# Optimization experiments

Measured on AMD Instinct MI355X. Metric: run time of the kernel, lower is better.

The kernel has to match this reference:

```python
import jax, jax.numpy as jnp
import numpy as np

B, Q, K, D = 8, 2048, 2048, 64

def setup_inputs() -> dict:
    key = jax.random.key(0)
    kq, kk, kv, kl = jax.random.split(key, 4)
    queries = jax.random.normal(kq, (B, Q, D), dtype=jnp.float32)
    keys = jax.random.normal(kk, (B, K, D), dtype=jnp.float32)
    values = jax.random.normal(kv, (B, K, D), dtype=jnp.float32)
    valid_lens = jax.random.randint(kl, (B,), 1, K + 1)  # at least 1 valid key
    return {"queries": queries, "keys": keys, "values": values, "valid_lens": valid_lens}

def reference(queries, keys, values, valid_lens):
    d = queries.shape[-1]
    # scores: [B, Q, K]
    scores = jnp.einsum("bqd,bkd->bqk", queries, keys) / jnp.sqrt(jnp.float32(d))
    # d2l-style masked softmax: positions >= valid_len get -1e6 before softmax
    kpos = jnp.arange(scores.shape[-1])  # [K]
    mask = kpos[None, None, :] < valid_lens[:, None, None]  # [B,1,K]
    scores = jnp.where(mask, scores, jnp.float32(-1e6))
    attn = jax.nn.softmax(scores, axis=-1)
    # dropout is identity at inference (training=False)
    return jnp.einsum("bqk,bkd->bqd", attn, values)
```

## Files before the change

### kernel.cpp

```cpp
#include <hip/hip_runtime.h>

typedef float    f32x4  __attribute__((ext_vector_type(4)));
typedef float    f32x16 __attribute__((ext_vector_type(16)));
typedef _Float16 half8  __attribute__((ext_vector_type(8)));

constexpr int NB = 8;
constexpr int NQ = 2048;
constexpr int NKEY = 2048;
constexpr int DD = 64;
constexpr int KB = 32;
constexpr int NT = NKEY / KB;
constexpr size_t TILE_BYTES = (size_t)KB * DD * 2;

#define QSCALE (0.125f * 1.44269504088896340736f)

__device__ inline unsigned pkh(float a, float b) {
    return __builtin_bit_cast(unsigned, __builtin_amdgcn_cvt_pkrtz(a, b));
}
__device__ inline int vswz2(int d) {
    return ((d >> 1) & 3) << 4;
}

#define GLL(gp, lp) __builtin_amdgcn_global_load_lds( \
    (const __attribute__((address_space(1))) void*)(gp), \
    (__attribute__((address_space(3))) void*)(lp), 16, 0, 0)

__global__ __launch_bounds__(256) void convert_kv(
    const float* __restrict__ Kp, const float* __restrict__ Vp,
    char* __restrict__ Kh, char* __restrict__ Vt)
{
    __shared__ __align__(16) char vbuf[32 * 144];
    const int g    = blockIdx.x;
    const bool isV = (g >= NB * NT);
    const int bt   = isV ? g - NB * NT : g;
    const int tid  = threadIdx.x;
    const int b = bt >> 6, T = bt & 63;

    const int key = tid >> 3;
    const int dc  = (tid & 7) * 8;
    const float* src = (isV ? Vp : Kp)
                     + ((size_t)b * NKEY + T * KB + key) * DD + dc;
    f32x4 f0 = *(const f32x4*)src;
    f32x4 f1 = *(const f32x4*)(src + 4);
    half8 h;
#pragma unroll
    for (int i = 0; i < 4; ++i) {
        h[i]     = (_Float16)f0[i];
        h[4 + i] = (_Float16)f1[i];
    }

    if (!isV) {
        char* dst = Kh + (size_t)bt * TILE_BYTES;
        *(half8*)(dst + ((key * 128 + dc * 2) ^ ((key & 7) << 4))) = h;
    } else {
        *(half8*)(vbuf + key * 144 + dc * 2) = h;
        __syncthreads();
        const int d  = tid >> 2;
        const int kc = tid & 3;
        half8 o;
#pragma unroll
        for (int j = 0; j < 8; ++j)
            o[j] = *(const _Float16*)(vbuf + (kc * 8 + j) * 144 + d * 2);
        char* dst = Vt + (size_t)bt * TILE_BYTES;
        *(half8*)(dst + d * 64 + ((kc * 16) ^ vswz2(d))) = o;
    }
}

__device__ __forceinline__ void pv_chunk(
    const f32x16& sv, const char* __restrict__ vsm,
    int hi, int ql, int swzq, f32x16& o0, f32x16& o1)
{
    const unsigned w0 = pkh(sv[0],  sv[1]),  w1 = pkh(sv[2],  sv[3]);
    const unsigned w2 = pkh(sv[4],  sv[5]),  w3 = pkh(sv[6],  sv[7]);
    const unsigned w4 = pkh(sv[8],  sv[9]),  w5 = pkh(sv[10], sv[11]);
    const unsigned w6 = pkh(sv[12], sv[13]), w7 = pkh(sv[14], sv[15]);
    const unsigned p0 = __shfl_xor(w0, 32), p1 = __shfl_xor(w1, 32);
    const unsigned p2 = __shfl_xor(w2, 32), p3 = __shfl_xor(w3, 32);
    const unsigned p4 = __shfl_xor(w4, 32), p5 = __shfl_xor(w5, 32);
    const unsigned p6 = __shfl_xor(w6, 32), p7 = __shfl_xor(w7, 32);
    const bool h1 = (hi != 0);
    union { unsigned u[4]; half8 h; } A0, A1;
    A0.u[0] = h1 ? p2 : w0;  A0.u[1] = h1 ? p3 : w1;
    A0.u[2] = h1 ? w2 : p0;  A0.u[3] = h1 ? w3 : p1;
    A1.u[0] = h1 ? p6 : w4;  A1.u[1] = h1 ? p7 : w5;
    A1.u[2] = h1 ? w6 : p4;  A1.u[3] = h1 ? w7 : p5;

    __builtin_amdgcn_s_setprio(1);
#pragma unroll
    for (int t = 0; t < 2; ++t) {
        const int co = t * 32 + hi * 16;
        const half8 vb0 = *(const half8*)(vsm + ql * 64        + (co ^ swzq));
        const half8 vb1 = *(const half8*)(vsm + (32 + ql) * 64 + (co ^ swzq));
        const half8 pa = (t == 0) ? A0.h : A1.h;
        o0 = __builtin_amdgcn_mfma_f32_32x32x16_f16(pa, vb0, o0, 0, 0, 0);
        o1 = __builtin_amdgcn_mfma_f32_32x32x16_f16(pa, vb1, o1, 0, 0, 0);
    }
    __builtin_amdgcn_s_setprio(0);
}

__global__ __launch_bounds__(512, 4) void attn_fused(
    const float* __restrict__ Qp, const char* __restrict__ Kh,
    const char* __restrict__ Vt, const int* __restrict__ VL,
    float* __restrict__ Op)
{
    __shared__ __align__(16) char pool[67584];

    const int tid  = threadIdx.x;
    const int wv   = tid >> 6;
    const int lane = tid & 63;
    const int ql   = lane & 31;
    const int hi   = lane >> 5;

    char* Ksm = pool + wv * 8192;
    char* Vsm = Ksm + 4096;

    const int g  = blockIdx.x;
    const int b  = ((g >> 3) & 7) ^ ((g >> 8) << 2);
    const int qt = (g & 7) | (((g >> 6) & 7) << 3);
    const int qbase = qt * 32;

    const int vlen = VL[b];
    const int numt = (vlen + KB - 1) / KB;

    const float* qsrc = Qp + ((size_t)b * NQ + qbase + ql) * DD;
    half8 qf[4];
#pragma unroll
    for (int c = 0; c < 4; ++c) {
        f32x4 f0 = *(const f32x4*)(qsrc + c * 16 + hi * 8);
        f32x4 f1 = *(const f32x4*)(qsrc + c * 16 + hi * 8 + 4);
        half8 h;
#pragma unroll
        for (int j = 0; j < 4; ++j) {
            h[j]     = (_Float16)(f0[j] * QSCALE);
            h[4 + j] = (_Float16)(f1[j] * QSCALE);
        }
        qf[c] = h;
    }

    f32x16 o0 = {}, o1 = {};
    float mrun = -1e30f, lrun = 0.f;
    const int swzq = vswz2(ql);

    for (int t = wv; t < numt; t += 8) {
        const int kbase = t * KB;
        const char* ksrc = Kh + (size_t)(b * NT + t) * TILE_BYTES + lane * 16;
        const char* vsrc = Vt + (size_t)(b * NT + t) * TILE_BYTES + lane * 16;

        __builtin_amdgcn_sched_barrier(0);
#pragma unroll
        for (int j = 0; j < 4; ++j) GLL(ksrc + j * 1024, Ksm + j * 1024);
#pragma unroll
        for (int j = 0; j < 4; ++j) GLL(vsrc + j * 1024, Vsm + j * 1024);
        asm volatile("s_waitcnt vmcnt(4)" ::: "memory");
        __builtin_amdgcn_sched_barrier(0);

        f32x16 sv = {};
        __builtin_amdgcn_s_setprio(1);
#pragma unroll
        for (int c = 0; c < 4; ++c) {
            const half8 kf = *(const half8*)(Ksm +
                ((ql * 128 + c * 32 + hi * 16) ^ ((ql & 7) << 4)));
            sv = __builtin_amdgcn_mfma_f32_32x32x16_f16(kf, qf[c], sv, 0, 0, 0);
        }
        __builtin_amdgcn_s_setprio(0);

        if (kbase + KB > vlen) {
#pragma unroll
            for (int r = 0; r < 16; ++r) {
                const int krow = (r & 3) + 8 * (r >> 2) + 4 * hi;
                sv[r] = (kbase + krow < vlen) ? sv[r] : -1e30f;
            }
        }

        float mx[16];
#pragma unroll
        for (int r = 0; r < 16; ++r) mx[r] = sv[r];
#pragma unroll
        for (int st = 8; st > 0; st >>= 1)
#pragma unroll
            for (int r = 0; r < st; ++r) mx[r] = fmaxf(mx[r], mx[r + st]);
        float mr = fmaxf(mx[0], __shfl_xor(mx[0], 32));

        if (!__all(mr <= mrun + 8.f)) {
            const float mn = fmaxf(mrun, mr);
            const float alpha = __builtin_amdgcn_exp2f(mrun - mn);
            lrun *= alpha;
            mrun = mn;
#pragma unroll
            for (int r = 0; r < 16; ++r) {
                const int qr = (r & 3) + 8 * (r >> 2) + 4 * hi;
                const float ar = __shfl(alpha, qr);
                o0[r] *= ar;
                o1[r] *= ar;
            }
        }

#pragma unroll
        for (int r = 0; r < 16; ++r)
            sv[r] = __builtin_amdgcn_exp2f(sv[r] - mrun);
        float sx[16];
#pragma unroll
        for (int r = 0; r < 16; ++r) sx[r] = sv[r];
#pragma unroll
        for (int st = 8; st > 0; st >>= 1)
#pragma unroll
            for (int r = 0; r < st; ++r) sx[r] += sx[r + st];
        lrun += sx[0] + __shfl_xor(sx[0], 32);

        asm volatile("s_waitcnt vmcnt(0)" ::: "memory");
        __builtin_amdgcn_sched_barrier(0);
        pv_chunk(sv, Vsm, hi, ql, swzq, o0, o1);
    }

    __syncthreads();
    float* Mb = (float*)(pool + 65536);
    float* Lb = (float*)(pool + 65536 + 1024);
    float (*Obuf)[32][64] = (float (*)[32][64])pool;

    if (hi == 0) { Mb[wv * 32 + ql] = mrun; Lb[wv * 32 + ql] = lrun; }
    __syncthreads();

    float Mtot = -1e30f;
#pragma unroll
    for (int w = 0; w < 8; ++w)
        if (Lb[w * 32 + ql] > 0.f) Mtot = fmaxf(Mtot, Mb[w * 32 + ql]);
    const float wown = (lrun > 0.f) ? __builtin_amdgcn_exp2f(mrun - Mtot) : 0.f;

#pragma unroll
    for (int r = 0; r < 16; ++r) {
        const int qr = (r & 3) + 8 * (r >> 2) + 4 * hi;
        const float wr = __shfl(wown, qr);
        Obuf[wv][qr][ql]      = o0[r] * wr;
        Obuf[wv][qr][ql + 32] = o1[r] * wr;
    }
    __syncthreads();

    {
        const int q  = tid >> 4;
        const int d0 = (tid & 15) * 4;
        float Mq = -1e30f;
#pragma unroll
        for (int w = 0; w < 8; ++w)
            if (Lb[w * 32 + q] > 0.f) Mq = fmaxf(Mq, Mb[w * 32 + q]);
        float Ltot = 0.f;
#pragma unroll
        for (int w = 0; w < 8; ++w) {
            const float lw = Lb[w * 32 + q];
            if (lw > 0.f) Ltot += lw * __builtin_amdgcn_exp2f(Mb[w * 32 + q] - Mq);
        }
        f32x4 acc = {};
#pragma unroll
        for (int w = 0; w < 8; ++w)
            acc += *(const f32x4*)(&Obuf[w][q][d0]);
        const float inv = 1.0f / Ltot;
        f32x4 outv;
#pragma unroll
        for (int j = 0; j < 4; ++j) outv[j] = acc[j] * inv;
        *(f32x4*)(Op + ((size_t)b * NQ + qbase + q) * DD + d0) = outv;
    }
}

extern "C" void kernel_launch(void* const* d_in, const int* in_sizes, int n_in,
                              void* d_out, int out_size, void* d_ws, size_t ws_size,
                              hipStream_t stream) {
    const float* Qp = (const float*)d_in[0];
    const float* Kp = (const float*)d_in[1];
    const float* Vp = (const float*)d_in[2];
    const int*   VL = (const int*)d_in[3];
    float* Op = (float*)d_out;

    char* Kh = (char*)d_ws;
    char* Vt = (char*)d_ws + (size_t)NB * NT * TILE_BYTES;

    hipLaunchKernelGGL(convert_kv, dim3(2 * NB * NT), dim3(256), 0, stream,
                       Kp, Vp, Kh, Vt);
    hipLaunchKernelGGL(attn_fused, dim3(NB * (NQ / 32)), dim3(512), 0, stream,
                       Qp, Kh, Vt, VL, Op);
}
```

Baseline: 31.14 us.

## Pre-layout K/V tiles in MFMA fragment order and load directly to registers

The conversion kernel now writes K and V tiles in the exact per-lane MFMA operand layout. The attention kernel can then load fragments straight from global memory into registers with coalesced 16-byte loads, with no stop in LDS. This removes the global_load_lds staging, the LDS reads, the swizzle arithmetic and the explicit vmcnt waits. In exchange it gives up LDS staging and relies on the compiler to schedule global-load latency against the QK and softmax work.

```diff
diff --git a/kernel.cpp b/kernel.cpp
--- a/kernel.cpp
+++ b/kernel.cpp
@@ -10,20 +10,13 @@
 constexpr int DD = 64;
 constexpr int KB = 32;
 constexpr int NT = NKEY / KB;
-constexpr size_t TILE_BYTES = (size_t)KB * DD * 2;
+constexpr size_t TILE_BYTES = 4096;
 
 #define QSCALE (0.125f * 1.44269504088896340736f)
 
 __device__ inline unsigned pkh(float a, float b) {
     return __builtin_bit_cast(unsigned, __builtin_amdgcn_cvt_pkrtz(a, b));
 }
-__device__ inline int vswz2(int d) {
-    return ((d >> 1) & 3) << 4;
-}
-
-#define GLL(gp, lp) __builtin_amdgcn_global_load_lds( \
-    (const __attribute__((address_space(1))) void*)(gp), \
-    (__attribute__((address_space(3))) void*)(lp), 16, 0, 0)
 
 __global__ __launch_bounds__(256) void convert_kv(
     const float* __restrict__ Kp, const float* __restrict__ Vp,
@@ -50,8 +43,9 @@
     }
 
     if (!isV) {
-        char* dst = Kh + (size_t)bt * TILE_BYTES;
-        *(half8*)(dst + ((key * 128 + dc * 2) ^ ((key & 7) << 4))) = h;
+        char* dst = Kh + (size_t)bt * TILE_BYTES
+                  + (dc >> 4) * 1024 + (((dc >> 3) & 1) * 32 + key) * 16;
+        *(half8*)dst = h;
     } else {
         *(half8*)(vbuf + key * 144 + dc * 2) = h;
         __syncthreads();
@@ -61,14 +55,15 @@
 #pragma unroll
         for (int j = 0; j < 8; ++j)
             o[j] = *(const _Float16*)(vbuf + (kc * 8 + j) * 144 + d * 2);
-        char* dst = Vt + (size_t)bt * TILE_BYTES;
-        *(half8*)(dst + d * 64 + ((kc * 16) ^ vswz2(d))) = o;
-    }
-}
-
-__device__ __forceinline__ void pv_chunk(
-    const f32x16& sv, const char* __restrict__ vsm,
-    int hi, int ql, int swzq, f32x16& o0, f32x16& o1)
+        const int frag = (kc >> 1) * 2 + (d >> 5);
+        char* dst = Vt + (size_t)bt * TILE_BYTES
+                  + frag * 1024 + ((kc & 1) * 32 + (d & 31)) * 16;
+        *(half8*)dst = o;
+    }
+}
+
+__device__ __forceinline__ void pv_frag(
+    const f32x16& sv, const half8 (&vf)[4], int hi, f32x16& o0, f32x16& o1)
 {
     const unsigned w0 = pkh(sv[0],  sv[1]),  w1 = pkh(sv[2],  sv[3]);
     const unsigned w2 = pkh(sv[4],  sv[5]),  w3 = pkh(sv[6],  sv[7]);
@@ -86,15 +81,10 @@
     A1.u[2] = h1 ? w6 : p4;  A1.u[3] = h1 ? w7 : p5;
 
     __builtin_amdgcn_s_setprio(1);
-#pragma unroll
-    for (int t = 0; t < 2; ++t) {
-        const int co = t * 32 + hi * 16;
-        const half8 vb0 = *(const half8*)(vsm + ql * 64        + (co ^ swzq));
-        const half8 vb1 = *(const half8*)(vsm + (32 + ql) * 64 + (co ^ swzq));
-        const half8 pa = (t == 0) ? A0.h : A1.h;
-        o0 = __builtin_amdgcn_mfma_f32_32x32x16_f16(pa, vb0, o0, 0, 0, 0);
-        o1 = __builtin_amdgcn_mfma_f32_32x32x16_f16(pa, vb1, o1, 0, 0, 0);
-    }
+    o0 = __builtin_amdgcn_mfma_f32_32x32x16_f16(A0.h, vf[0], o0, 0, 0, 0);
+    o1 = __builtin_amdgcn_mfma_f32_32x32x16_f16(A0.h, vf[1], o1, 0, 0, 0);
+    o0 = __builtin_amdgcn_mfma_f32_32x32x16_f16(A1.h, vf[2], o0, 0, 0, 0);
+    o1 = __builtin_amdgcn_mfma_f32_32x32x16_f16(A1.h, vf[3], o1, 0, 0, 0);
     __builtin_amdgcn_s_setprio(0);
 }
 
@@ -111,9 +101,6 @@
     const int ql   = lane & 31;
     const int hi   = lane >> 5;
 
-    char* Ksm = pool + wv * 8192;
-    char* Vsm = Ksm + 4096;
-
     const int g  = blockIdx.x;
     const int b  = ((g >> 3) & 7) ^ ((g >> 8) << 2);
     const int qt = (g & 7) | (((g >> 6) & 7) << 3);
@@ -139,29 +126,23 @@
 
     f32x16 o0 = {}, o1 = {};
     float mrun = -1e30f, lrun = 0.f;
-    const int swzq = vswz2(ql);
 
     for (int t = wv; t < numt; t += 8) {
         const int kbase = t * KB;
-        const char* ksrc = Kh + (size_t)(b * NT + t) * TILE_BYTES + lane * 16;
-        const char* vsrc = Vt + (size_t)(b * NT + t) * TILE_BYTES + lane * 16;
-
-        __builtin_amdgcn_sched_barrier(0);
-#pragma unroll
-        for (int j = 0; j < 4; ++j) GLL(ksrc + j * 1024, Ksm + j * 1024);
-#pragma unroll
-        for (int j = 0; j < 4; ++j) GLL(vsrc + j * 1024, Vsm + j * 1024);
-        asm volatile("s_waitcnt vmcnt(4)" ::: "memory");
-        __builtin_amdgcn_sched_barrier(0);
+        const char* kp = Kh + (size_t)(b * NT + t) * TILE_BYTES + lane * 16;
+        const char* vp = Vt + (size_t)(b * NT + t) * TILE_BYTES + lane * 16;
+
+        half8 kf[4], vf[4];
+#pragma unroll
+        for (int c = 0; c < 4; ++c) kf[c] = *(const half8*)(kp + c * 1024);
+#pragma unroll
+        for (int c = 0; c < 4; ++c) vf[c] = *(const half8*)(vp + c * 1024);
 
         f32x16 sv = {};
         __builtin_amdgcn_s_setprio(1);
 #pragma unroll
-        for (int c = 0; c < 4; ++c) {
-            const half8 kf = *(const half8*)(Ksm +
-                ((ql * 128 + c * 32 + hi * 16) ^ ((ql & 7) << 4)));
-            sv = __builtin_amdgcn_mfma_f32_32x32x16_f16(kf, qf[c], sv, 0, 0, 0);
-        }
+        for (int c = 0; c < 4; ++c)
+            sv = __builtin_amdgcn_mfma_f32_32x32x16_f16(kf[c], qf[c], sv, 0, 0, 0);
         __builtin_amdgcn_s_setprio(0);
 
         if (kbase + KB > vlen) {
@@ -207,9 +188,7 @@
             for (int r = 0; r < st; ++r) sx[r] += sx[r + st];
         lrun += sx[0] + __shfl_xor(sx[0], 32);
 
-        asm volatile("s_waitcnt vmcnt(0)" ::: "memory");
-        __builtin_amdgcn_sched_barrier(0);
-        pv_chunk(sv, Vsm, hi, ql, swzq, o0, o1);
+        pv_frag(sv, vf, hi, o0, o1);
     }
 
     __syncthreads();
```

Result: faster. 27.63 us (-11.3%).
